# Optimization experiments

Measured on AMD Instinct MI355X. Metric: run time of the kernel, lower is better.

The kernel has to match this reference:

```python
import math
import jax, jax.numpy as jnp
from jax import lax
import numpy as np

RADIUS = 6
K = 2 * RADIUS + 1  # 13


def _conv(x, w, b, stride):
    # torch Conv2d(kernel=3, padding=1)
    y = lax.conv_general_dilated(
        x, w, window_strides=(stride, stride), padding=((1, 1), (1, 1)),
        dimension_numbers=("NCHW", "OIHW", "NCHW"))
    return y + b[None, :, None, None]


def _encoder(x, w1, b1, w2, b2, w3, b3):
    x = jax.nn.relu(_conv(x, w1, b1, 1))
    x = jax.nn.relu(_conv(x, w2, b2, 2))
    x = jax.nn.relu(_conv(x, w3, b3, 2))
    return x  # [B,128,H/4,W/4]


def _local_corr(z_t, z_t1):
    # Equivalent to unfold(z_t1, K, pad=RADIUS) -> multiply z_t -> sum over C,
    # but computed per-offset to avoid materializing [B,C,K*K,H,W].
    B, C, H, W = z_t.shape
    zp = jnp.pad(z_t1, ((0, 0), (0, 0), (RADIUS, RADIUS), (RADIUS, RADIUS)))
    inv_sqrt_c = 1.0 / np.sqrt(C).astype(np.float32)
    # unfold flattening order is (ki, kj) row-major, matching this loop order
    slabs = [
        (z_t * zp[:, :, i:i + H, j:j + W]).sum(axis=1)
        for i in range(K) for j in range(K)
    ]
    return jnp.stack(slabs, axis=1) * inv_sqrt_c  # [B, K*K, H, W]


def setup_inputs() -> dict:
    key = jax.random.key(0)
    ks = jax.random.split(key, 10)
    f32 = jnp.float32

    def w_init(k, shape, fan_in):
        return jax.random.normal(k, shape, dtype=f32) * np.sqrt(2.0 / fan_in).astype(np.float32)

    return {
        "img_t": jax.random.normal(ks[0], (32, 3, 256, 256), dtype=f32),
        "img_t1": jax.random.normal(ks[1], (32, 3, 256, 256), dtype=f32),
        "w1": w_init(ks[2], (32, 3, 3, 3), 3 * 9),
        "b1": jnp.zeros((32,), dtype=f32),
        "w2": w_init(ks[3], (64, 32, 3, 3), 32 * 9),
        "b2": jnp.zeros((64,), dtype=f32),
        "w3": w_init(ks[4], (128, 64, 3, 3), 64 * 9),
        "b3": jnp.zeros((128,), dtype=f32),
        "w_head": w_init(ks[5], (2, K * K), K * K),
        "b_head": jnp.zeros((2,), dtype=f32),
    }


def reference(img_t, img_t1, w1, b1, w2, b2, w3, b3, w_head, b_head):
    z_t = _encoder(img_t, w1, b1, w2, b2, w3, b3)
    z_t1 = _encoder(img_t1, w1, b1, w2, b2, w3, b3)
    corr = _local_corr(z_t, z_t1)          # [B, 169, H/4, W/4]
    h_t = corr.mean(axis=(2, 3))           # [B, 169]
    pred = h_t @ w_head.T + b_head         # [B, 2]
    return (pred, z_t, z_t1, corr, h_t)
```

## Files before the change

### kernel.cpp

```cpp
#include <hip/hip_runtime.h>

typedef _Float16 f16;
typedef _Float16 h4 __attribute__((ext_vector_type(4)));
typedef _Float16 v8h __attribute__((ext_vector_type(8)));
typedef _Float16 h8 __attribute__((ext_vector_type(8)));
typedef float v4f __attribute__((ext_vector_type(4)));

#define INV_SQRT_C 0.08838834764831845f

__global__ void wt1_k(const float* __restrict__ w1, f16* __restrict__ wT)
{
  int idx = blockIdx.x * 256 + threadIdx.x;
  int k = idx & 31, row = idx >> 5;
  float v = 0.f;
  if (row < 32) {
    int oc = row, q = k >> 3, j = k & 7;
    if (q < 3) v = w1[(oc * 3 + q) * 9 + j];
  } else {
    int oc = row - 32;
    if (k < 3) v = w1[(oc * 3 + k) * 9 + 8];
  }
  wT[idx] = (f16)v;
}

__global__ void wt2_k(const float* __restrict__ w2, f16* __restrict__ wT)
{
  int idx = blockIdx.x * 256 + threadIdx.x;
  int ic = idx & 31, oc = (idx >> 5) & 63, khkw = idx >> 11;
  wT[idx] = (f16)w2[(oc * 32 + ic) * 9 + khkw];
}

__global__ void wt3_k(const float* __restrict__ w3, f16* __restrict__ wT)
{
  int idx = blockIdx.x * 256 + threadIdx.x;
  int ic5 = idx & 31, oc = (idx >> 5) & 127, ch = idx >> 12;
  int khkw = ch >> 1, ich = ch & 1;
  int ic = ich * 32 + ic5;
  wT[idx] = (f16)w3[(oc * 64 + ic) * 9 + khkw];
}

__global__ __launch_bounds__(256, 4) void conv12_m(const float* __restrict__ img_t,
    const float* __restrict__ img_t1,
    const f16* __restrict__ wT1, const float* __restrict__ b1,
    const f16* __restrict__ wT2, const float* __restrict__ b2, f16* __restrict__ out)
{
  const int oh = blockIdx.x, g = blockIdx.y, bb = blockIdx.z;
  const int tid = threadIdx.x;
  const int lane = tid & 63, wv = tid >> 6;
  const int n15 = lane & 15, quad = lane >> 4;

  __shared__ f16 sImgF[5][134][4];
  __shared__ f16 sA[3 * 132 * 40];

  const int OW0 = g * 64;
  const int ibase = 2 * OW0 - 2;
  const int ihb = 2 * oh - 2;
  const float* imgb = (bb < 32 ? img_t : img_t1) + (long)(bb & 31) * 3 * 65536;

  {
    float gld[3][3];
    int colA[3], rA[3];
    bool okA[3];
    #pragma unroll
    for (int i = 0; i < 3; i++) {
      int p = tid + i * 256;
      bool pok = p < 670;
      int pc = pok ? p : 0;
      int col = pc % 134, r = pc / 134;
      int ih = ihb + r, iw = ibase + col;
      bool ok = pok && ((unsigned)ih < 256u) && ((unsigned)iw < 256u);
      const float* rp = imgb + ih * 256 + iw;
      gld[i][0] = ok ? rp[0] : 0.f;
      gld[i][1] = ok ? rp[65536] : 0.f;
      gld[i][2] = ok ? rp[131072] : 0.f;
      colA[i] = col; rA[i] = r; okA[i] = pok;
    }
    #pragma unroll
    for (int i = 0; i < 3; i++) {
      if (okA[i]) {
        h4 pk;
        pk[0] = (f16)gld[i][0]; pk[1] = (f16)gld[i][1];
        pk[2] = (f16)gld[i][2]; pk[3] = (f16)0.f;
        *(h4*)(&sImgF[rA[i]][colA[i]][0]) = pk;
      }
    }
  }
  __syncthreads();

  v8h a0 = *(const v8h*)(wT1 + n15 * 32 + quad * 8);
  v8h a1 = *(const v8h*)(wT1 + (16 + n15) * 32 + quad * 8);
  v8h a2 = *(const v8h*)(wT1 + (32 + n15) * 32 + quad * 8);
  v8h a3 = *(const v8h*)(wT1 + (48 + n15) * 32 + quad * 8);
  float4 bb0 = *(const float4*)(b1 + quad * 4);
  float4 bb1 = *(const float4*)(b1 + 16 + quad * 4);

  for (int grp = wv; grp < 25; grp += 4) {
    int p = grp * 16 + n15;
    bool pv = p < 387;
    int pc = pv ? p : 386;
    int yr = pc >= 258 ? 2 : (pc >= 129 ? 1 : 0);
    int ci = pc - yr * 129;
    const f16* sp = &sImgF[yr][ci][0] + quad;
    v8h B1;
    #pragma unroll
    for (int j = 0; j < 8; j++)
      B1[j] = sp[(j / 3) * 536 + (j % 3) * 4];
    h4 t = *(const h4*)(&sImgF[yr + 2][ci + 2][0]);
    v8h B2;
    B2[0] = t[0]; B2[1] = t[1]; B2[2] = t[2]; B2[3] = t[3];
    B2[4] = t[0]; B2[5] = t[1]; B2[6] = t[2]; B2[7] = t[3];
    v4f acc0 = {}, acc1 = {};
    acc0 = __builtin_amdgcn_mfma_f32_16x16x32_f16(a0, B1, acc0, 0, 0, 0);
    acc1 = __builtin_amdgcn_mfma_f32_16x16x32_f16(a1, B1, acc1, 0, 0, 0);
    acc0 = __builtin_amdgcn_mfma_f32_16x16x32_f16(a2, B2, acc0, 0, 0, 0);
    acc1 = __builtin_amdgcn_mfma_f32_16x16x32_f16(a3, B2, acc1, 0, 0, 0);
    int y = 2 * oh - 1 + yr;
    int iw = ibase + 1 + ci;
    bool valid = pv && ((unsigned)y < 256u) && ((unsigned)iw < 256u);
    f16* base = &sA[(yr * 132 + ci) * 40];
    h4 pk0, pk1;
    #pragma unroll
    for (int r = 0; r < 4; r++) {
      float v0 = acc0[r] + ((const float*)&bb0)[r];
      float v1 = acc1[r] + ((const float*)&bb1)[r];
      pk0[r] = (f16)((valid && v0 > 0.f) ? v0 : 0.f);
      pk1[r] = (f16)((valid && v1 > 0.f) ? v1 : 0.f);
    }
    if (pv) {
      *(h4*)(base + quad * 4) = pk0;
      *(h4*)(base + 16 + quad * 4) = pk1;
    }
  }
  __syncthreads();

  v4f acc[4] = {};
  for (int kh = 0; kh < 3; kh++) {
    for (int kw = 0; kw < 3; kw++) {
      int khkw = kh * 3 + kw;
      const f16* wp = wT2 + khkw * 2048 + n15 * 32 + quad * 8;
      v8h w0 = *(const v8h*)(wp);
      v8h w1v = *(const v8h*)(wp + 512);
      v8h w2v = *(const v8h*)(wp + 1024);
      v8h w3v = *(const v8h*)(wp + 1536);
      int ci = 32 * wv + 2 * n15 + kw;
      v8h bf = *(const v8h*)&sA[(kh * 132 + ci) * 40 + quad * 8];
      acc[0] = __builtin_amdgcn_mfma_f32_16x16x32_f16(w0, bf, acc[0], 0, 0, 0);
      acc[1] = __builtin_amdgcn_mfma_f32_16x16x32_f16(w1v, bf, acc[1], 0, 0, 0);
      acc[2] = __builtin_amdgcn_mfma_f32_16x16x32_f16(w2v, bf, acc[2], 0, 0, 0);
      acc[3] = __builtin_amdgcn_mfma_f32_16x16x32_f16(w3v, bf, acc[3], 0, 0, 0);
    }
  }
  const int ow = OW0 + wv * 16 + n15;
  #pragma unroll
  for (int mt = 0; mt < 4; mt++) {
    int oc0 = mt * 16 + quad * 4;
    float4 bbv = *(const float4*)(b2 + oc0);
    h4 pk;
    #pragma unroll
    for (int r = 0; r < 4; r++) {
      float v = acc[mt][r] + ((const float*)&bbv)[r];
      pk[r] = (f16)(v > 0.f ? v : 0.f);
    }
    *(h4*)(out + (((long)(bb * 128 + oh) * 128 + ow) * 64) + oc0) = pk;
  }
}

__global__ __launch_bounds__(256, 3) void conv3_m(const f16* __restrict__ in,
    const f16* __restrict__ wT, const float* __restrict__ b3,
    float* __restrict__ zbase, f16* __restrict__ nhbase)
{
  const int oh = blockIdx.x, bb = blockIdx.y;
  const int ib = bb >> 5, b = bb & 31;
  const int tid = threadIdx.x;
  const int lane = tid & 63, wv = tid >> 6;
  const int n15 = lane & 15, quad = lane >> 4;
  const int ow = wv * 16 + n15;

  __shared__ f16 sIn[3 * 128 * 64];

  const f16* inb = in + (long)bb * (128 * 128 * 64);
  const int ih0 = 2 * oh - 1;

  {
    h8 stg[12];
    #pragma unroll
    for (int i = 0; i < 12; i++) {
      int idx = tid + i * 256;
      int ck = idx & 7, iw = (idx >> 3) & 127, r = idx >> 10;
      int ih = ih0 + r;
      h8 v;
      #pragma unroll
      for (int e = 0; e < 8; e++) v[e] = (f16)0.f;
      if ((unsigned)ih < 128u) v = *(const h8*)(inb + ((long)(ih * 128 + iw)) * 64 + ck * 8);
      stg[i] = v;
    }
    #pragma unroll
    for (int i = 0; i < 12; i++) {
      int idx = tid + i * 256;
      int ck = idx & 7, iw = (idx >> 3) & 127, r = idx >> 10;
      int sck = ck ^ ((iw >> 1) & 7);
      *(h8*)(&sIn[(r * 128 + iw) * 64 + sck * 8]) = stg[i];
    }
  }
  __syncthreads();

  v4f acc[8] = {};
  for (int kh = 0; kh < 3; kh++) {
    for (int kw = 0; kw < 3; kw++) {
      int iw = 2 * ow + kw - 1;
      bool bok = (unsigned)iw < 128u;
      int iwc = bok ? iw : 0;
      #pragma unroll
      for (int ich = 0; ich < 2; ich++) {
        int ch = (kh * 3 + kw) * 2 + ich;
        int ck = ich * 4 + quad;
        int sck = ck ^ ((iwc >> 1) & 7);
        v8h bf;
        #pragma unroll
        for (int e = 0; e < 8; e++) bf[e] = (f16)0.f;
        if (bok) bf = *(const v8h*)&sIn[(kh * 128 + iwc) * 64 + sck * 8];
        const f16* wp = wT + ((long)(ch * 128 + n15)) * 32 + quad * 8;
        #pragma unroll
        for (int mt = 0; mt < 8; mt++) {
          v8h a = *(const v8h*)(wp + mt * 512);
          acc[mt] = __builtin_amdgcn_mfma_f32_16x16x32_f16(a, bf, acc[mt], 0, 0, 0);
        }
      }
    }
  }

  float* zo = zbase + (long)ib * 16777216L;
  f16* nh = nhbase + (long)ib * 16777216L;
  #pragma unroll
  for (int mt = 0; mt < 8; mt++) {
    int oc0 = mt * 16 + quad * 4;
    float4 bbv = *(const float4*)(b3 + oc0);
    float rv[4];
    #pragma unroll
    for (int r = 0; r < 4; r++) {
      float v = acc[mt][r] + ((const float*)&bbv)[r];
      rv[r] = v > 0.f ? v : 0.f;
    }
    #pragma unroll
    for (int r = 0; r < 4; r++)
      zo[(((long)(b * 128 + oc0 + r) * 64 + oh) * 64) + ow] = rv[r];
    h4 pk;
    #pragma unroll
    for (int r = 0; r < 4; r++) pk[r] = (f16)rv[r];
    *(h4*)(nh + (((long)(b * 64 + oh) * 64 + ow) * 128) + oc0) = pk;
  }
}

__global__ __launch_bounds__(256) void corr_m(const f16* __restrict__ zt,
    const f16* __restrict__ zt1, float* __restrict__ corr, float* __restrict__ part)
{
  const int h = blockIdx.x, b = blockIdx.y;
  const int lane = threadIdx.x & 63, wv = threadIdx.x >> 6;
  const int n15 = lane & 15, quad = lane >> 4;
  const int w0 = wv * 16;
  __shared__ float sC[64][17];

  const f16* arow = zt + (((long)(b * 64 + h) * 64 + (w0 + n15)) * 128) + quad * 8;
  v8h A[4];
  #pragma unroll
  for (int ks = 0; ks < 4; ks++) A[ks] = *(const v8h*)(arow + ks * 32);

  float* cb = corr + (long)b * 169 * 4096 + h * 64;

  const int q4r0 = quad * 4;
  const int wq0 = w0 - 6 + n15;
  const int wq1 = w0 + 10 + n15;
  const bool ok0 = (unsigned)wq0 < 64u;
  const bool ok1 = (unsigned)wq1 < 64u;

  for (int ki = 0; ki < 13; ki++) {
    int row = h + ki - 6;
    bool rok = (unsigned)row < 64u;
    v4f acc0 = {}, acc1 = {};
    if (rok) {
      const f16* brow = zt1 + ((long)(b * 64 + row) * 64) * 128;
      const f16* bp0 = brow + (long)wq0 * 128 + quad * 8;
      const f16* bp1 = brow + (long)wq1 * 128 + quad * 8;
      #pragma unroll
      for (int ks = 0; ks < 4; ks++) {
        v8h b0, b1;
        #pragma unroll
        for (int k = 0; k < 8; k++) { b0[k] = (f16)0.f; b1[k] = (f16)0.f; }
        if (ok0) b0 = *(const v8h*)(bp0 + ks * 32);
        if (ok1) b1 = *(const v8h*)(bp1 + ks * 32);
        acc0 = __builtin_amdgcn_mfma_f32_16x16x32_f16(A[ks], b0, acc0, 0, 0, 0);
        acc1 = __builtin_amdgcn_mfma_f32_16x16x32_f16(A[ks], b1, acc1, 0, 0, 0);
      }
    }
    __syncthreads();
    #pragma unroll
    for (int r = 0; r < 4; r++) {
      int q4r = q4r0 + r;
      int w = w0 + q4r;
      int kj0 = n15 - q4r;
      if (kj0 >= 0 && kj0 < 13) sC[w][kj0] = acc0[r] * INV_SQRT_C;
      int kj1 = kj0 + 16;
      if (kj1 < 13) sC[w][kj1] = acc1[r] * INV_SQRT_C;
    }
    __syncthreads();
    for (int idx = threadIdx.x; idx < 832; idx += 256) {
      int w = idx & 63, kj = idx >> 6;
      float v = sC[w][kj];
      cb[(long)(ki * 13 + kj) * 4096 + w] = v;
      #pragma unroll
      for (int off = 32; off > 0; off >>= 1) v += __shfl_down(v, off, 64);
      if (lane == 0) part[(long)(ki * 13 + kj) * 2048 + b * 64 + h] = v;
    }
  }
}

__global__ __launch_bounds__(256) void ht2_k(const float* __restrict__ part,
                                             float* __restrict__ ht)
{
  int o = blockIdx.x;
  int t = threadIdx.x;
  int b = t >> 3, s = t & 7;
  const float* p = part + (long)o * 2048 + b * 64 + s * 8;
  float v = 0.f;
  #pragma unroll
  for (int i = 0; i < 8; i++) v += p[i];
  #pragma unroll
  for (int off = 4; off > 0; off >>= 1) v += __shfl_down(v, off, 8);
  if (s == 0) ht[b * 169 + o] = v * (1.f / 4096.f);
}

__global__ void pred_k(const float* __restrict__ ht, const float* __restrict__ wh,
                       const float* __restrict__ bh, float* __restrict__ pred)
{
  int t = threadIdx.x;
  int b = t >> 1, j = t & 1;
  float s = bh[j];
  for (int o = 0; o < 169; o++) s = fmaf(ht[b * 169 + o], wh[j * 169 + o], s);
  pred[b * 2 + j] = s;
}

extern "C" void kernel_launch(void* const* d_in, const int* in_sizes, int n_in,
                              void* d_out, int out_size, void* d_ws, size_t ws_size,
                              hipStream_t stream)
{
  (void)in_sizes; (void)n_in; (void)out_size; (void)ws_size;
  const float* img_t  = (const float*)d_in[0];
  const float* img_t1 = (const float*)d_in[1];
  const float* w1 = (const float*)d_in[2];
  const float* b1 = (const float*)d_in[3];
  const float* w2 = (const float*)d_in[4];
  const float* b2 = (const float*)d_in[5];
  const float* w3 = (const float*)d_in[6];
  const float* b3 = (const float*)d_in[7];
  const float* wh = (const float*)d_in[8];
  const float* bh = (const float*)d_in[9];
  float* out = (float*)d_out;

  char* ws = (char*)d_ws;
  f16* bufB = (f16*)ws;
  f16* nhT  = (f16*)(ws + 134217728L);
  float* part = (float*)(ws + 201326592L);

  const long OUT_ZT   = 64;
  const long OUT_ZT1  = OUT_ZT + 16777216L;
  const long OUT_CORR = OUT_ZT1 + 16777216L;
  const long OUT_HT   = OUT_CORR + 22151168L;

  f16* wT1 = (f16*)(out + OUT_CORR);
  f16* wT2 = wT1 + 2048;
  f16* wT3 = wT2 + 18432;

  wt1_k<<<8, 256, 0, stream>>>(w1, wT1);
  wt2_k<<<72, 256, 0, stream>>>(w2, wT2);
  wt3_k<<<288, 256, 0, stream>>>(w3, wT3);

  conv12_m<<<dim3(128, 2, 64), 256, 0, stream>>>(img_t, img_t1, wT1, b1, wT2, b2, bufB);
  conv3_m<<<dim3(64, 64), 256, 0, stream>>>(bufB, wT3, b3, out + OUT_ZT, nhT);
  corr_m<<<dim3(64, 32), 256, 0, stream>>>(nhT, nhT + 16777216L, out + OUT_CORR, part);
  ht2_k<<<169, 256, 0, stream>>>(part, out + OUT_HT);
  pred_k<<<1, 64, 0, stream>>>(out + OUT_HT, wh, bh, out);
}
```

Measured before the change: 740.7 us.

## Process eight output rows per conv12 block with register-prefetched double-buffered input

Each conv12 block now loops over eight consecutive output rows instead of one, cutting the grid to 16 row-chunks. The image tile for the next row is loaded from global memory into registers before the current row's compute and written into a second LDS buffer afterwards, which hides global load latency and amortises per-block setup and weight loads. Adjacent rows still reload overlapping input rows rather than reusing them. The trade-off is fewer blocks (2048 instead of 16384), less parallelism for hiding latency across blocks, and more register pressure from the prefetch state.

```diff
diff --git a/kernel.cpp b/kernel.cpp
--- a/kernel.cpp
+++ b/kernel.cpp
@@ -39,53 +39,58 @@
   wT[idx] = (f16)w3[(oc * 64 + ic) * 9 + khkw];
 }
 
+#define STAGE_ISSUE(OH)                                                     \
+  {                                                                         \
+    int ihb_ = 2 * (OH) - 2;                                                \
+    _Pragma("unroll")                                                       \
+    for (int i = 0; i < 3; i++) {                                           \
+      int ih = ihb_ + rS[i], iw = ibase + colS[i];                          \
+      bool ok = pokS[i] && ((unsigned)ih < 256u) && ((unsigned)iw < 256u);  \
+      const float* rp = imgb + ih * 256 + iw;                               \
+      g0[i] = ok ? rp[0] : 0.f;                                             \
+      g1[i] = ok ? rp[65536] : 0.f;                                         \
+      g2[i] = ok ? rp[131072] : 0.f;                                        \
+    }                                                                       \
+  }
+
+#define STAGE_WRITE(BUF)                                                    \
+  {                                                                         \
+    _Pragma("unroll")                                                       \
+    for (int i = 0; i < 3; i++) {                                           \
+      if (pokS[i]) {                                                        \
+        h4 pk;                                                              \
+        pk[0] = (f16)g0[i]; pk[1] = (f16)g1[i];                             \
+        pk[2] = (f16)g2[i]; pk[3] = (f16)0.f;                               \
+        *(h4*)(&sImgF[BUF][rS[i]][colS[i]][0]) = pk;                        \
+      }                                                                     \
+    }                                                                       \
+  }
+
 __global__ __launch_bounds__(256, 4) void conv12_m(const float* __restrict__ img_t,
     const float* __restrict__ img_t1,
     const f16* __restrict__ wT1, const float* __restrict__ b1,
     const f16* __restrict__ wT2, const float* __restrict__ b2, f16* __restrict__ out)
 {
-  const int oh = blockIdx.x, g = blockIdx.y, bb = blockIdx.z;
+  const int ohc = blockIdx.x, g = blockIdx.y, bb = blockIdx.z;
   const int tid = threadIdx.x;
   const int lane = tid & 63, wv = tid >> 6;
   const int n15 = lane & 15, quad = lane >> 4;
 
-  __shared__ f16 sImgF[5][134][4];
+  __shared__ f16 sImgF[2][5][134][4];
   __shared__ f16 sA[3 * 132 * 40];
 
   const int OW0 = g * 64;
   const int ibase = 2 * OW0 - 2;
-  const int ihb = 2 * oh - 2;
   const float* imgb = (bb < 32 ? img_t : img_t1) + (long)(bb & 31) * 3 * 65536;
 
-  {
-    float gld[3][3];
-    int colA[3], rA[3];
-    bool okA[3];
-    #pragma unroll
-    for (int i = 0; i < 3; i++) {
-      int p = tid + i * 256;
-      bool pok = p < 670;
-      int pc = pok ? p : 0;
-      int col = pc % 134, r = pc / 134;
-      int ih = ihb + r, iw = ibase + col;
-      bool ok = pok && ((unsigned)ih < 256u) && ((unsigned)iw < 256u);
-      const float* rp = imgb + ih * 256 + iw;
-      gld[i][0] = ok ? rp[0] : 0.f;
-      gld[i][1] = ok ? rp[65536] : 0.f;
-      gld[i][2] = ok ? rp[131072] : 0.f;
-      colA[i] = col; rA[i] = r; okA[i] = pok;
-    }
-    #pragma unroll
-    for (int i = 0; i < 3; i++) {
-      if (okA[i]) {
-        h4 pk;
-        pk[0] = (f16)gld[i][0]; pk[1] = (f16)gld[i][1];
-        pk[2] = (f16)gld[i][2]; pk[3] = (f16)0.f;
-        *(h4*)(&sImgF[rA[i]][colA[i]][0]) = pk;
-      }
-    }
-  }
-  __syncthreads();
+  int colS[3], rS[3]; bool pokS[3];
+  #pragma unroll
+  for (int i = 0; i < 3; i++) {
+    int p = tid + i * 256;
+    pokS[i] = p < 670;
+    int pc = pokS[i] ? p : 0;
+    colS[i] = pc % 134; rS[i] = pc / 134;
+  }
 
   v8h a0 = *(const v8h*)(wT1 + n15 * 32 + quad * 8);
   v8h a1 = *(const v8h*)(wT1 + (16 + n15) * 32 + quad * 8);
@@ -94,74 +99,89 @@
   float4 bb0 = *(const float4*)(b1 + quad * 4);
   float4 bb1 = *(const float4*)(b1 + 16 + quad * 4);
 
-  for (int grp = wv; grp < 25; grp += 4) {
-    int p = grp * 16 + n15;
-    bool pv = p < 387;
-    int pc = pv ? p : 386;
-    int yr = pc >= 258 ? 2 : (pc >= 129 ? 1 : 0);
-    int ci = pc - yr * 129;
-    const f16* sp = &sImgF[yr][ci][0] + quad;
-    v8h B1;
-    #pragma unroll
-    for (int j = 0; j < 8; j++)
-      B1[j] = sp[(j / 3) * 536 + (j % 3) * 4];
-    h4 t = *(const h4*)(&sImgF[yr + 2][ci + 2][0]);
-    v8h B2;
-    B2[0] = t[0]; B2[1] = t[1]; B2[2] = t[2]; B2[3] = t[3];
-    B2[4] = t[0]; B2[5] = t[1]; B2[6] = t[2]; B2[7] = t[3];
-    v4f acc0 = {}, acc1 = {};
-    acc0 = __builtin_amdgcn_mfma_f32_16x16x32_f16(a0, B1, acc0, 0, 0, 0);
-    acc1 = __builtin_amdgcn_mfma_f32_16x16x32_f16(a1, B1, acc1, 0, 0, 0);
-    acc0 = __builtin_amdgcn_mfma_f32_16x16x32_f16(a2, B2, acc0, 0, 0, 0);
-    acc1 = __builtin_amdgcn_mfma_f32_16x16x32_f16(a3, B2, acc1, 0, 0, 0);
-    int y = 2 * oh - 1 + yr;
-    int iw = ibase + 1 + ci;
-    bool valid = pv && ((unsigned)y < 256u) && ((unsigned)iw < 256u);
-    f16* base = &sA[(yr * 132 + ci) * 40];
-    h4 pk0, pk1;
-    #pragma unroll
-    for (int r = 0; r < 4; r++) {
-      float v0 = acc0[r] + ((const float*)&bb0)[r];
-      float v1 = acc1[r] + ((const float*)&bb1)[r];
-      pk0[r] = (f16)((valid && v0 > 0.f) ? v0 : 0.f);
-      pk1[r] = (f16)((valid && v1 > 0.f) ? v1 : 0.f);
-    }
-    if (pv) {
-      *(h4*)(base + quad * 4) = pk0;
-      *(h4*)(base + 16 + quad * 4) = pk1;
-    }
-  }
-  __syncthreads();
-
-  v4f acc[4] = {};
-  for (int kh = 0; kh < 3; kh++) {
-    for (int kw = 0; kw < 3; kw++) {
-      int khkw = kh * 3 + kw;
-      const f16* wp = wT2 + khkw * 2048 + n15 * 32 + quad * 8;
-      v8h w0 = *(const v8h*)(wp);
-      v8h w1v = *(const v8h*)(wp + 512);
-      v8h w2v = *(const v8h*)(wp + 1024);
-      v8h w3v = *(const v8h*)(wp + 1536);
-      int ci = 32 * wv + 2 * n15 + kw;
-      v8h bf = *(const v8h*)&sA[(kh * 132 + ci) * 40 + quad * 8];
-      acc[0] = __builtin_amdgcn_mfma_f32_16x16x32_f16(w0, bf, acc[0], 0, 0, 0);
-      acc[1] = __builtin_amdgcn_mfma_f32_16x16x32_f16(w1v, bf, acc[1], 0, 0, 0);
-      acc[2] = __builtin_amdgcn_mfma_f32_16x16x32_f16(w2v, bf, acc[2], 0, 0, 0);
-      acc[3] = __builtin_amdgcn_mfma_f32_16x16x32_f16(w3v, bf, acc[3], 0, 0, 0);
-    }
-  }
-  const int ow = OW0 + wv * 16 + n15;
-  #pragma unroll
-  for (int mt = 0; mt < 4; mt++) {
-    int oc0 = mt * 16 + quad * 4;
-    float4 bbv = *(const float4*)(b2 + oc0);
-    h4 pk;
-    #pragma unroll
-    for (int r = 0; r < 4; r++) {
-      float v = acc[mt][r] + ((const float*)&bbv)[r];
-      pk[r] = (f16)(v > 0.f ? v : 0.f);
-    }
-    *(h4*)(out + (((long)(bb * 128 + oh) * 128 + ow) * 64) + oc0) = pk;
+  float g0[3], g1[3], g2[3];
+  const int oh0 = ohc * 8;
+
+  STAGE_ISSUE(oh0);
+  STAGE_WRITE(0);
+
+  for (int it = 0; it < 8; it++) {
+    const int oh = oh0 + it;
+    const int cur = it & 1;
+    if (it < 7) STAGE_ISSUE(oh + 1);
+    __syncthreads();
+
+    for (int grp = wv; grp < 25; grp += 4) {
+      int p = grp * 16 + n15;
+      bool pv = p < 387;
+      int pc = pv ? p : 386;
+      int yr = pc >= 258 ? 2 : (pc >= 129 ? 1 : 0);
+      int ci = pc - yr * 129;
+      const f16* sp = &sImgF[cur][yr][ci][0] + quad;
+      v8h B1;
+      #pragma unroll
+      for (int j = 0; j < 8; j++)
+        B1[j] = sp[(j / 3) * 536 + (j % 3) * 4];
+      h4 t = *(const h4*)(&sImgF[cur][yr + 2][ci + 2][0]);
+      v8h B2;
+      B2[0] = t[0]; B2[1] = t[1]; B2[2] = t[2]; B2[3] = t[3];
+      B2[4] = t[0]; B2[5] = t[1]; B2[6] = t[2]; B2[7] = t[3];
+      v4f acc0 = {}, acc1 = {};
+      acc0 = __builtin_amdgcn_mfma_f32_16x16x32_f16(a0, B1, acc0, 0, 0, 0);
+      acc1 = __builtin_amdgcn_mfma_f32_16x16x32_f16(a1, B1, acc1, 0, 0, 0);
+      acc0 = __builtin_amdgcn_mfma_f32_16x16x32_f16(a2, B2, acc0, 0, 0, 0);
+      acc1 = __builtin_amdgcn_mfma_f32_16x16x32_f16(a3, B2, acc1, 0, 0, 0);
+      int y = 2 * oh - 1 + yr;
+      int iw = ibase + 1 + ci;
+      bool valid = pv && ((unsigned)y < 256u) && ((unsigned)iw < 256u);
+      f16* base = &sA[(yr * 132 + ci) * 40];
+      h4 pk0, pk1;
+      #pragma unroll
+      for (int r = 0; r < 4; r++) {
+        float v0 = acc0[r] + ((const float*)&bb0)[r];
+        float v1 = acc1[r] + ((const float*)&bb1)[r];
+        pk0[r] = (f16)((valid && v0 > 0.f) ? v0 : 0.f);
+        pk1[r] = (f16)((valid && v1 > 0.f) ? v1 : 0.f);
+      }
+      if (pv) {
+        *(h4*)(base + quad * 4) = pk0;
+        *(h4*)(base + 16 + quad * 4) = pk1;
+      }
+    }
+    __syncthreads();
+
+    v4f acc[4] = {};
+    for (int kh = 0; kh < 3; kh++) {
+      for (int kw = 0; kw < 3; kw++) {
+        int khkw = kh * 3 + kw;
+        const f16* wp = wT2 + khkw * 2048 + n15 * 32 + quad * 8;
+        v8h w0 = *(const v8h*)(wp);
+        v8h w1v = *(const v8h*)(wp + 512);
+        v8h w2v = *(const v8h*)(wp + 1024);
+        v8h w3v = *(const v8h*)(wp + 1536);
+        int ci = 32 * wv + 2 * n15 + kw;
+        v8h bf = *(const v8h*)&sA[(kh * 132 + ci) * 40 + quad * 8];
+        acc[0] = __builtin_amdgcn_mfma_f32_16x16x32_f16(w0, bf, acc[0], 0, 0, 0);
+        acc[1] = __builtin_amdgcn_mfma_f32_16x16x32_f16(w1v, bf, acc[1], 0, 0, 0);
+        acc[2] = __builtin_amdgcn_mfma_f32_16x16x32_f16(w2v, bf, acc[2], 0, 0, 0);
+        acc[3] = __builtin_amdgcn_mfma_f32_16x16x32_f16(w3v, bf, acc[3], 0, 0, 0);
+      }
+    }
+    const int ow = OW0 + wv * 16 + n15;
+    #pragma unroll
+    for (int mt = 0; mt < 4; mt++) {
+      int oc0 = mt * 16 + quad * 4;
+      float4 bbv = *(const float4*)(b2 + oc0);
+      h4 pk;
+      #pragma unroll
+      for (int r = 0; r < 4; r++) {
+        float v = acc[mt][r] + ((const float*)&bbv)[r];
+        pk[r] = (f16)(v > 0.f ? v : 0.f);
+      }
+      *(h4*)(out + (((long)(bb * 128 + oh) * 128 + ow) * 64) + oc0) = pk;
+    }
+
+    if (it < 7) STAGE_WRITE(cur ^ 1);
   }
 }
 
@@ -374,7 +394,7 @@
   wt2_k<<<72, 256, 0, stream>>>(w2, wT2);
   wt3_k<<<288, 256, 0, stream>>>(w3, wT3);
 
-  conv12_m<<<dim3(128, 2, 64), 256, 0, stream>>>(img_t, img_t1, wT1, b1, wT2, b2, bufB);
+  conv12_m<<<dim3(16, 2, 64), 256, 0, stream>>>(img_t, img_t1, wT1, b1, wT2, b2, bufB);
   conv3_m<<<dim3(64, 64), 256, 0, stream>>>(bufB, wT3, b3, out + OUT_ZT, nhT);
   corr_m<<<dim3(64, 32), 256, 0, stream>>>(nhT, nhT + 16777216L, out + OUT_CORR, part);
   ht2_k<<<169, 256, 0, stream>>>(part, out + OUT_HT);
```

Measured after the change: 681.3 us. 8.0% less time.
